# Optimization experiments

Measured on AMD Instinct MI355X. Metric: run time of the kernel, lower is better.

Reference implementation:

```python
import jax, jax.numpy as jnp
import numpy as np

D = 512
NPRE = NMLP = NPOST = 16
TOPK = 8
P = NPRE * NMLP * NPOST
HMAX = 5 * D  # max MLP expert hidden (j//4 up to 3 -> 2+3=5)
B, S = 1, 256


def _gelu(x):
    return jax.nn.gelu(x, approximate=False)  # torch nn.GELU default (erf)


def _ln(x, g, b, eps=1e-5):
    m = x.mean(-1, keepdims=True)
    v = ((x - m) ** 2).mean(-1, keepdims=True)
    return (x - m) / jnp.sqrt(v + eps) * g + b


def setup_inputs() -> dict:
    key = jax.random.key(0)
    ks = iter(jax.random.split(key, 16))
    w = lambda shape: jax.random.normal(next(ks), shape, jnp.float32) * 0.02
    inp = {"x": jax.random.normal(next(ks), (B, S, D), jnp.float32)}
    # router: Linear(D,256)->GELU->Linear(256,128)->GELU->Linear(128,P); dropout off (eval)
    inp["Wr1"] = w((D, 256)); inp["br1"] = jnp.zeros((256,), jnp.float32)
    inp["Wr2"] = w((256, 128)); inp["br2"] = jnp.zeros((128,), jnp.float32)
    inp["Wr3"] = w((128, P)); inp["br3"] = jnp.zeros((P,), jnp.float32)
    inp["temp"] = jnp.ones((1,), jnp.float32)
    # pre experts: Linear(D,D) + LayerNorm + {GELU,ReLU,Tanh} by i%3
    inp["Wpre"] = w((NPRE, D, D)); inp["bpre"] = jnp.zeros((NPRE, D), jnp.float32)
    inp["gpre"] = jnp.ones((NPRE, D), jnp.float32); inp["bpre_ln"] = jnp.zeros((NPRE, D), jnp.float32)
    # mlp experts: heterogeneous hidden D*(2+j//4), zero-padded to HMAX
    W1 = np.zeros((NMLP, D, HMAX), np.float32)
    b1 = np.zeros((NMLP, HMAX), np.float32)
    W2 = np.zeros((NMLP, HMAX, D), np.float32)
    rng = np.random.default_rng(0)
    for j in range(NMLP):
        h = D * (2 + j // 4)
        W1[j, :, :h] = rng.normal(0.0, 0.02, (D, h)).astype(np.float32)
        W2[j, :h, :] = rng.normal(0.0, 0.02, (h, D)).astype(np.float32)
    inp["W1"] = jnp.asarray(W1); inp["b1"] = jnp.asarray(b1)
    inp["W2"] = jnp.asarray(W2); inp["b2"] = jnp.zeros((NMLP, D), jnp.float32)
    # post experts: Linear(D,D) + (LayerNorm if p%2==0); dropout off (eval)
    inp["Wpost"] = w((NPOST, D, D)); inp["bpost"] = jnp.zeros((NPOST, D), jnp.float32)
    inp["gpost"] = jnp.ones((NPOST, D), jnp.float32); inp["bpost_ln"] = jnp.zeros((NPOST, D), jnp.float32)
    return inp


def _forward(x, Wr1, br1, Wr2, br2, Wr3, br3, temp,
             Wpre, bpre, gpre, bpre_ln, W1, b1, W2, b2,
             Wpost, bpost, gpost, bpost_ln):
    b, s, _ = x.shape
    # ---- router ----
    h = _gelu(x @ Wr1 + br1)
    h = _gelu(h @ Wr2 + br2)
    scores = h @ Wr3 + br3  # [B,S,P]
    # ---- GLBL loss (torch.var -> unbiased, ddof=1) ----
    freq = jax.nn.softmax(scores, axis=-1).mean((0, 1))  # [P]
    var = jnp.sum((freq - freq.mean()) ** 2) / (P - 1)
    glbl_loss = P * var
    # ---- top-k routing ----
    probs = jax.nn.softmax(scores / temp, axis=-1)
    top_vals, top_idx = jax.lax.top_k(probs, TOPK)  # [B,S,K]
    bb = jnp.arange(b)[:, None, None]
    ss = jnp.arange(s)[None, :, None]
    pw = jnp.zeros_like(probs).at[bb, ss, top_idx].set(top_vals)
    pw = pw / (pw.sum(-1, keepdims=True) + 1e-8)  # diagnostic pathway_weights
    # ---- decompose pathway index -> (pre, mlp, post) ----
    pre_i = top_idx // (NMLP * NPOST)
    rem = top_idx % (NMLP * NPOST)
    mlp_i = rem // NPOST
    post_i = rem % NPOST
    # ---- pre experts: compute all, gather per slot ----
    pre_lin = jnp.einsum('bsd,edf->bsef', x, Wpre) + bpre  # [B,S,E,D]
    pre_ln = _ln(pre_lin, gpre, bpre_ln)
    aid = (jnp.arange(NPRE) % 3)[:, None]  # [E,1] broadcast over D
    pre_all = jnp.where(aid == 0, _gelu(pre_ln),
                        jnp.where(aid == 1, jax.nn.relu(pre_ln), jnp.tanh(pre_ln)))
    x_pre = jnp.take_along_axis(pre_all, pre_i[..., None], axis=2)  # [B,S,K,D]
    # ---- mlp experts: heterogeneous hidden, dense compute + mask-combine ----
    mlp_out = jnp.zeros_like(x_pre)
    for j in range(NMLP):
        hd = D * (2 + j // 4)
        hj = x_pre @ W1[j, :, :hd] + b1[j, :hd]
        hj = _gelu(hj) if j % 2 == 0 else jax.nn.relu(hj)
        yj = hj @ W2[j, :hd, :] + b2[j]
        mlp_out = mlp_out + jnp.where((mlp_i == j)[..., None], yj, 0.0)
    # ---- post experts ----
    post_out = jnp.zeros_like(mlp_out)
    for p in range(NPOST):
        yp = mlp_out @ Wpost[p] + bpost[p]
        if p % 2 == 0:
            yp = _ln(yp, gpost[p], bpost_ln[p])
        post_out = post_out + jnp.where((post_i == p)[..., None], yp, 0.0)
    # ---- weighted sum over slots (original uses raw top-k probs as weights) ----
    output = jnp.einsum('bsk,bskd->bsd', top_vals, post_out)
    return output, glbl_loss, pw


def reference(x, Wr1, br1, Wr2, br2, Wr3, br3, temp,
              Wpre, bpre, gpre, bpre_ln, W1, b1, W2, b2,
              Wpost, bpost, gpost, bpost_ln):
    return _forward(x, Wr1, br1, Wr2, br2, Wr3, br3, temp,
                    Wpre, bpre, gpre, bpre_ln, W1, b1, W2, b2,
                    Wpost, bpost, gpost, bpost_ln)
```

## Files before the change

### kernel.cpp

```cpp
#include <hip/hip_runtime.h>
#include <math.h>

#define S 256
#define D 512
#define P 4096
#define TOPK 8
#define NPAIR (S*TOPK)
#define HMAX 2560

#define OFF_H1     0
#define OFF_H2     65536
#define OFF_SCORES 98304
#define OFF_PROBS  1146880
#define OFF_TOPV   2195456
#define OFF_TOPI   2197504
#define OFF_CNT    2199552
#define OFF_LP     2199616
#define OFF_LM     2232384
#define OFF_LQ     2265152
#define OFF_PRE    2297920
#define OFF_HBUF   3346496
#define OFF_MLPO   8589376
#define OFF_POSTL  9637952
#define OFF_FREQ   10686528


__device__ __forceinline__ float geluf(float x) {
    return 0.5f * x * (1.0f + erff(x * 0.70710678118654752440f));
}

__device__ __forceinline__ float blockReduceSum(float v, float* red, int tid) {
    __syncthreads();
    #pragma unroll
    for (int o = 32; o; o >>= 1) v += __shfl_down(v, o);
    if ((tid & 63) == 0) red[tid >> 6] = v;
    __syncthreads();
    return red[0] + red[1] + red[2] + red[3];
}

__device__ __forceinline__ float blockReduceMax(float v, float* red, int tid) {
    __syncthreads();
    #pragma unroll
    for (int o = 32; o; o >>= 1) v = fmaxf(v, __shfl_down(v, o));
    if ((tid & 63) == 0) red[tid >> 6] = v;
    __syncthreads();
    return fmaxf(fmaxf(red[0], red[1]), fmaxf(red[2], red[3]));
}

__global__ __launch_bounds__(256) void gemm_grouped(
    const float* __restrict__ A, int lda, int amode,
    const int* __restrict__ list, int listStride,
    const int* __restrict__ counts, int fixedM,
    const float* __restrict__ W, long long wStride, int ldw,
    const float* __restrict__ bias, int biasStride,
    float* __restrict__ C, int ldc,
    int N, int K, int hetN, int hetK, int act)
{
    int e = blockIdx.z;
    int he = 512 * (2 + (e >> 2));
    int Ne = hetN ? he : N;
    int Ke = hetK ? he : K;
    int Me = counts ? counts[e] : fixedM;
    int row0 = blockIdx.y * 64; if (row0 >= Me) return;
    int col0 = blockIdx.x * 64; if (col0 >= Ne) return;

    const float* We = W + (long long)e * wStride + col0;
    const float* be = bias + (size_t)e * biasStride + col0;
    const int* le = list ? (list + (size_t)e * listStride) : nullptr;

    __shared__ float As[64][36];
    __shared__ float Ws[32][68];

    int tid = threadIdx.x;
    int laR = tid >> 3, laK = (tid & 7) << 2;
    int lwK = tid >> 4, lwC = (tid & 15) << 2;

    const float* aptr0 = nullptr; const float* aptr1 = nullptr;
    {
        int r = row0 + laR;
        if (r < Me) { int ri = le ? le[r] : r; if (amode) ri >>= 3; aptr0 = A + (size_t)ri * lda + laK; }
        r = row0 + laR + 32;
        if (r < Me) { int ri = le ? le[r] : r; if (amode) ri >>= 3; aptr1 = A + (size_t)ri * lda + laK; }
    }

    float acc[4][4] = {};
    int tr = (tid >> 4) << 2, tc = (tid & 15) << 2;

    for (int k0 = 0; k0 < Ke; k0 += 32) {
        float4 v0 = make_float4(0.f, 0.f, 0.f, 0.f);
        float4 v1 = v0;
        if (aptr0) v0 = *(const float4*)(aptr0 + k0);
        if (aptr1) v1 = *(const float4*)(aptr1 + k0);
        *(float4*)&As[laR][laK] = v0;
        *(float4*)&As[laR + 32][laK] = v1;

        float4 w0 = *(const float4*)(We + (size_t)(k0 + lwK) * ldw + lwC);
        float4 w1 = *(const float4*)(We + (size_t)(k0 + lwK + 16) * ldw + lwC);
        *(float4*)&Ws[lwK][lwC] = w0;
        *(float4*)&Ws[lwK + 16][lwC] = w1;
        __syncthreads();

        #pragma unroll
        for (int kk = 0; kk < 32; kk++) {
            float a0 = As[tr][kk], a1 = As[tr + 1][kk], a2 = As[tr + 2][kk], a3 = As[tr + 3][kk];
            float b0 = Ws[kk][tc], b1 = Ws[kk][tc + 1], b2 = Ws[kk][tc + 2], b3 = Ws[kk][tc + 3];
            acc[0][0] += a0 * b0; acc[0][1] += a0 * b1; acc[0][2] += a0 * b2; acc[0][3] += a0 * b3;
            acc[1][0] += a1 * b0; acc[1][1] += a1 * b1; acc[1][2] += a1 * b2; acc[1][3] += a1 * b3;
            acc[2][0] += a2 * b0; acc[2][1] += a2 * b1; acc[2][2] += a2 * b2; acc[2][3] += a2 * b3;
            acc[3][0] += a3 * b0; acc[3][1] += a3 * b1; acc[3][2] += a3 * b2; acc[3][3] += a3 * b3;
        }
        __syncthreads();
    }

    int ae = act;
    if (act == 3) ae = (e & 1) ? 2 : 1;
    #pragma unroll
    for (int i = 0; i < 4; i++) {
        int r = row0 + tr + i;
        if (r >= Me) continue;
        int crow = le ? le[r] : r;
        float* Cr = C + (size_t)crow * ldc + col0 + tc;
        #pragma unroll
        for (int j = 0; j < 4; j++) {
            float v = acc[i][j] + be[tc + j];
            if (ae == 1) v = geluf(v);
            else if (ae == 2) v = fmaxf(v, 0.f);
            Cr[j] = v;
        }
    }
}

__global__ __launch_bounds__(256) void softmax_topk_kernel(
    const float* __restrict__ scores, const float* __restrict__ temp,
    float* __restrict__ probs, float* __restrict__ topv, int* __restrict__ topi,
    float* __restrict__ pw)
{
    __shared__ float s[P];
    __shared__ float red[8];
    __shared__ float lv[256];
    __shared__ int   li[256];
    __shared__ float tvS[TOPK];
    __shared__ int   tiS[TOPK];

    int t = blockIdx.x, tid = threadIdx.x;
    const float* srow = scores + (size_t)t * P;

    float loc[16];
    #pragma unroll
    for (int j = 0; j < 16; j++) { loc[j] = srow[tid + 256 * j]; }

    float m = -1e30f;
    #pragma unroll
    for (int j = 0; j < 16; j++) m = fmaxf(m, loc[j]);
    m = blockReduceMax(m, red, tid);

    float invT = 1.0f / temp[0];
    float p1[16], pT[16];
    float s1 = 0.f, sT = 0.f;
    #pragma unroll
    for (int j = 0; j < 16; j++) {
        float d = loc[j] - m;
        p1[j] = expf(d);        s1 += p1[j];
        pT[j] = expf(d * invT); sT += pT[j];
    }
    s1 = blockReduceSum(s1, red, tid);
    sT = blockReduceSum(sT, red, tid);

    float iZ1 = 1.f / s1;
    float* prow = probs + (size_t)t * P;
    float* pwrow = pw + (size_t)t * P;
    #pragma unroll
    for (int j = 0; j < 16; j++) {
        int i = tid + 256 * j;
        prow[i] = p1[j] * iZ1;
        s[i] = pT[j];
        pwrow[i] = 0.f;
    }
    __syncthreads();

    for (int it = 0; it < TOPK; it++) {
        float bv = -1e30f; int bi = -1;
        #pragma unroll
        for (int j = 0; j < 16; j++) {
            int i = tid + 256 * j;
            float v = s[i];
            if (v > bv) { bv = v; bi = i; }
        }
        lv[tid] = bv; li[tid] = bi;
        __syncthreads();
        for (int st = 128; st; st >>= 1) {
            if (tid < st) {
                float ov = lv[tid + st]; int oi = li[tid + st];
                if (ov > lv[tid] || (ov == lv[tid] && oi < li[tid])) { lv[tid] = ov; li[tid] = oi; }
            }
            __syncthreads();
        }
        if (tid == 0) { tvS[it] = lv[0]; tiS[it] = li[0]; s[li[0]] = -1e30f; }
        __syncthreads();
    }

    if (tid == 0) {
        float iZT = 1.f / sT;
        float tvn[TOPK]; float ssum = 0.f;
        #pragma unroll
        for (int it = 0; it < TOPK; it++) { tvn[it] = tvS[it] * iZT; ssum += tvn[it]; }
        float inv = 1.f / (ssum + 1e-8f);
        #pragma unroll
        for (int it = 0; it < TOPK; it++) {
            int pair = t * TOPK + it;
            topv[pair] = tvn[it];
            topi[pair] = tiS[it];
            pwrow[tiS[it]] = tvn[it] * inv;
        }
    }
}

__global__ void freq_kernel(const float* __restrict__ probs, float* __restrict__ freq) {
    int p = blockIdx.x * 256 + threadIdx.x;
    float sum = 0.f;
    for (int t = 0; t < S; t++) sum += probs[(size_t)t * P + p];
    freq[p] = sum * (1.f / (float)S);
}

__global__ __launch_bounds__(256) void glbl_kernel(const float* __restrict__ freq, float* __restrict__ outLoss) {
    __shared__ float red[8];
    int tid = threadIdx.x;
    float sum = 0.f;
    #pragma unroll
    for (int j = 0; j < 16; j++) sum += freq[tid + 256 * j];
    float tot = blockReduceSum(sum, red, tid);
    float mean = tot * (1.f / (float)P);
    float q = 0.f;
    #pragma unroll
    for (int j = 0; j < 16; j++) { float d = freq[tid + 256 * j] - mean; q += d * d; }
    float sq = blockReduceSum(q, red, tid);
    if (tid == 0) outLoss[0] = (float)P * (sq / (float)(P - 1));
}

__global__ void zero_cnt_kernel(int* cnt) {
    if (threadIdx.x < 64) cnt[threadIdx.x] = 0;
}

__global__ void build_lists_kernel(const int* __restrict__ topi, int* cnt,
                                   int* lp, int* lm, int* lq) {
    int pair = blockIdx.x * 256 + threadIdx.x;
    if (pair >= NPAIR) return;
    int idx = topi[pair];
    int pre = idx >> 8, rem = idx & 255, ml = rem >> 4, po = rem & 15;
    int pos;
    pos = atomicAdd(&cnt[pre], 1);      lp[pre * NPAIR + pos] = pair;
    pos = atomicAdd(&cnt[16 + ml], 1);  lm[ml * NPAIR + pos] = pair;
    pos = atomicAdd(&cnt[32 + po], 1);  lq[po * NPAIR + pos] = pair;
}

__global__ __launch_bounds__(256) void pre_lnact_kernel(
    float* __restrict__ preOut, const int* __restrict__ topi,
    const float* __restrict__ g, const float* __restrict__ b)
{
    __shared__ float red[8];
    int pair = blockIdx.x, tid = threadIdx.x;
    int e = topi[pair] >> 8;
    float* row = preOut + (size_t)pair * D;
    float v0 = row[tid], v1 = row[tid + 256];
    float sm = blockReduceSum(v0 + v1, red, tid) * (1.f / (float)D);
    float d0 = v0 - sm, d1 = v1 - sm;
    float vv = blockReduceSum(d0 * d0 + d1 * d1, red, tid) * (1.f / (float)D);
    float rs = rsqrtf(vv + 1e-5f);
    v0 = d0 * rs * g[e * D + tid]       + b[e * D + tid];
    v1 = d1 * rs * g[e * D + tid + 256] + b[e * D + tid + 256];
    int a = e % 3;
    if (a == 0)      { v0 = geluf(v0);      v1 = geluf(v1); }
    else if (a == 1) { v0 = fmaxf(v0, 0.f); v1 = fmaxf(v1, 0.f); }
    else             { v0 = tanhf(v0);      v1 = tanhf(v1); }
    row[tid] = v0; row[tid + 256] = v1;
}

__global__ __launch_bounds__(256) void combine_kernel(
    const float* __restrict__ postLin, const float* __restrict__ topv,
    const int* __restrict__ topi, const float* __restrict__ g,
    const float* __restrict__ b, float* __restrict__ out)
{
    __shared__ float red[8];
    int t = blockIdx.x, tid = threadIdx.x;
    float a0 = 0.f, a1 = 0.f;
    for (int sl = 0; sl < TOPK; sl++) {
        int pair = t * TOPK + sl;
        int e = topi[pair] & 15;
        float tv = topv[pair];
        const float* row = postLin + (size_t)pair * D;
        float v0 = row[tid], v1 = row[tid + 256];
        if ((e & 1) == 0) {
            float sm = blockReduceSum(v0 + v1, red, tid) * (1.f / (float)D);
            float d0 = v0 - sm, d1 = v1 - sm;
            float vv = blockReduceSum(d0 * d0 + d1 * d1, red, tid) * (1.f / (float)D);
            float rs = rsqrtf(vv + 1e-5f);
            v0 = d0 * rs * g[e * D + tid]       + b[e * D + tid];
            v1 = d1 * rs * g[e * D + tid + 256] + b[e * D + tid + 256];
        }
        a0 += tv * v0; a1 += tv * v1;
    }
    out[(size_t)t * D + tid] = a0;
    out[(size_t)t * D + tid + 256] = a1;
}

extern "C" void kernel_launch(void* const* d_in, const int* in_sizes, int n_in,
                              void* d_out, int out_size, void* d_ws, size_t ws_size,
                              hipStream_t stream) {
    const float* x    = (const float*)d_in[0];
    const float* Wr1  = (const float*)d_in[1];
    const float* br1  = (const float*)d_in[2];
    const float* Wr2  = (const float*)d_in[3];
    const float* br2  = (const float*)d_in[4];
    const float* Wr3  = (const float*)d_in[5];
    const float* br3  = (const float*)d_in[6];
    const float* temp = (const float*)d_in[7];
    const float* Wpre = (const float*)d_in[8];
    const float* bpre = (const float*)d_in[9];
    const float* gpre = (const float*)d_in[10];
    const float* bpre_ln = (const float*)d_in[11];
    const float* W1   = (const float*)d_in[12];
    const float* b1   = (const float*)d_in[13];
    const float* W2   = (const float*)d_in[14];
    const float* b2   = (const float*)d_in[15];
    const float* Wpost = (const float*)d_in[16];
    const float* bpost = (const float*)d_in[17];
    const float* gpost = (const float*)d_in[18];
    const float* bpost_ln = (const float*)d_in[19];

    float* ws = (float*)d_ws;
    float* h1     = ws + OFF_H1;
    float* h2     = ws + OFF_H2;
    float* scores = ws + OFF_SCORES;
    float* probs  = ws + OFF_PROBS;
    float* topv   = ws + OFF_TOPV;
    int*   topi   = (int*)(ws + OFF_TOPI);
    int*   cnt    = (int*)(ws + OFF_CNT);
    int*   lp     = (int*)(ws + OFF_LP);
    int*   lm     = (int*)(ws + OFF_LM);
    int*   lq     = (int*)(ws + OFF_LQ);
    float* preOut = ws + OFF_PRE;
    float* Hbuf   = ws + OFF_HBUF;
    float* mlpOut = ws + OFF_MLPO;
    float* postLin = ws + OFF_POSTL;
    float* freq   = ws + OFF_FREQ;

    float* out   = (float*)d_out;
    float* outLoss = out + S * D;
    float* pw    = out + S * D + 1;

    hipLaunchKernelGGL(zero_cnt_kernel, dim3(1), dim3(64), 0, stream, cnt);

    hipLaunchKernelGGL(gemm_grouped, dim3(4, 4, 1), dim3(256), 0, stream,
        x, D, 0, (const int*)nullptr, 0, (const int*)nullptr, S,
        Wr1, 0LL, 256, br1, 0, h1, 256, 256, 512, 0, 0, 1);
    hipLaunchKernelGGL(gemm_grouped, dim3(2, 4, 1), dim3(256), 0, stream,
        h1, 256, 0, (const int*)nullptr, 0, (const int*)nullptr, S,
        Wr2, 0LL, 128, br2, 0, h2, 128, 128, 256, 0, 0, 1);
    hipLaunchKernelGGL(gemm_grouped, dim3(64, 4, 1), dim3(256), 0, stream,
        h2, 128, 0, (const int*)nullptr, 0, (const int*)nullptr, S,
        Wr3, 0LL, P, br3, 0, scores, P, P, 128, 0, 0, 0);

    hipLaunchKernelGGL(softmax_topk_kernel, dim3(S), dim3(256), 0, stream,
        scores, temp, probs, topv, topi, pw);

    hipLaunchKernelGGL(freq_kernel, dim3(16), dim3(256), 0, stream, probs, freq);
    hipLaunchKernelGGL(glbl_kernel, dim3(1), dim3(256), 0, stream, freq, outLoss);

    hipLaunchKernelGGL(build_lists_kernel, dim3(8), dim3(256), 0, stream, topi, cnt, lp, lm, lq);

    hipLaunchKernelGGL(gemm_grouped, dim3(8, 32, 16), dim3(256), 0, stream,
        x, D, 1, lp, NPAIR, cnt, 0,
        Wpre, (long long)D * D, D, bpre, D, preOut, D, D, D, 0, 0, 0);
    hipLaunchKernelGGL(pre_lnact_kernel, dim3(NPAIR), dim3(256), 0, stream,
        preOut, topi, gpre, bpre_ln);

    hipLaunchKernelGGL(gemm_grouped, dim3(40, 32, 16), dim3(256), 0, stream,
        preOut, D, 0, lm, NPAIR, cnt + 16, 0,
        W1, (long long)D * HMAX, HMAX, b1, HMAX, Hbuf, HMAX, 0, D, 1, 0, 3);
    hipLaunchKernelGGL(gemm_grouped, dim3(8, 32, 16), dim3(256), 0, stream,
        Hbuf, HMAX, 0, lm, NPAIR, cnt + 16, 0,
        W2, (long long)HMAX * D, D, b2, D, mlpOut, D, D, 0, 0, 1, 0);

    hipLaunchKernelGGL(gemm_grouped, dim3(8, 32, 16), dim3(256), 0, stream,
        mlpOut, D, 0, lq, NPAIR, cnt + 32, 0,
        Wpost, (long long)D * D, D, bpost, D, postLin, D, D, D, 0, 0, 0);

    hipLaunchKernelGGL(combine_kernel, dim3(S), dim3(256), 0, stream,
        postLin, topv, topi, gpost, bpost_ln, out);
}
```

Measured before the change: 773.6 us.

## Rewrite grouped GEMM with persistent work queue, async LDS double buffering, fused freq

```diff
diff --git a/kernel.cpp b/kernel.cpp
--- a/kernel.cpp
+++ b/kernel.cpp
@@ -11,24 +11,34 @@
 #define OFF_H1     0
 #define OFF_H2     65536
 #define OFF_SCORES 98304
-#define OFF_PROBS  1146880
-#define OFF_TOPV   2195456
-#define OFF_TOPI   2197504
-#define OFF_CNT    2199552
-#define OFF_LP     2199616
-#define OFF_LM     2232384
-#define OFF_LQ     2265152
-#define OFF_PRE    2297920
-#define OFF_HBUF   3346496
-#define OFF_MLPO   8589376
-#define OFF_POSTL  9637952
-#define OFF_FREQ   10686528
+#define OFF_TOPV   1146880
+#define OFF_TOPI   1148928
+#define OFF_CNT    1150976
+#define OFF_LP     1151040
+#define OFF_LM     1183808
+#define OFF_LQ     1216576
+#define OFF_PRE    1249344
+#define OFF_HBUF   2297920
+#define OFF_MLPO   7540800
+#define OFF_POSTL  8589376
+#define OFF_FREQ   9637952
+#define OFF_NIT    9642048
+#define OFF_QPRE   9642052
+#define OFF_QM1    9644100
+#define OFF_QM2    9652292
+#define OFF_QPOST  9654340
 
 
 __device__ __forceinline__ float geluf(float x) {
     return 0.5f * x * (1.0f + erff(x * 0.70710678118654752440f));
 }
 
+__device__ __forceinline__ void async_copy16(float* lds, const float* g) {
+    __builtin_amdgcn_global_load_lds(
+        (const __attribute__((address_space(1))) unsigned int*)g,
+        (__attribute__((address_space(3))) unsigned int*)lds, 16, 0, 0);
+}
+
 __device__ __forceinline__ float blockReduceSum(float v, float* red, int tid) {
     __syncthreads();
     #pragma unroll
@@ -47,92 +57,134 @@
     return fmaxf(fmaxf(red[0], red[1]), fmaxf(red[2], red[3]));
 }
 
-__global__ __launch_bounds__(256) void gemm_grouped(
+__global__ __launch_bounds__(256) void gemm_tile(
     const float* __restrict__ A, int lda, int amode,
-    const int* __restrict__ list, int listStride,
-    const int* __restrict__ counts, int fixedM,
+    const int* __restrict__ lists, const int* __restrict__ cnt,
+    const int4* __restrict__ queue, const int* __restrict__ nItemsPtr, int stageIdx,
+    int denseNB, int denseM,
     const float* __restrict__ W, long long wStride, int ldw,
     const float* __restrict__ bias, int biasStride,
-    float* __restrict__ C, int ldc,
-    int N, int K, int hetN, int hetK, int act)
+    float* __restrict__ C, int ldc, int K, int hetK, int act)
 {
-    int e = blockIdx.z;
-    int he = 512 * (2 + (e >> 2));
-    int Ne = hetN ? he : N;
-    int Ke = hetK ? he : K;
-    int Me = counts ? counts[e] : fixedM;
-    int row0 = blockIdx.y * 64; if (row0 >= Me) return;
-    int col0 = blockIdx.x * 64; if (col0 >= Ne) return;
-
-    const float* We = W + (long long)e * wStride + col0;
-    const float* be = bias + (size_t)e * biasStride + col0;
-    const int* le = list ? (list + (size_t)e * listStride) : nullptr;
-
-    __shared__ float As[64][36];
-    __shared__ float Ws[32][68];
-
-    int tid = threadIdx.x;
-    int laR = tid >> 3, laK = (tid & 7) << 2;
-    int lwK = tid >> 4, lwC = (tid & 15) << 2;
-
-    const float* aptr0 = nullptr; const float* aptr1 = nullptr;
-    {
-        int r = row0 + laR;
-        if (r < Me) { int ri = le ? le[r] : r; if (amode) ri >>= 3; aptr0 = A + (size_t)ri * lda + laK; }
-        r = row0 + laR + 32;
-        if (r < Me) { int ri = le ? le[r] : r; if (amode) ri >>= 3; aptr1 = A + (size_t)ri * lda + laK; }
-    }
-
-    float acc[4][4] = {};
-    int tr = (tid >> 4) << 2, tc = (tid & 15) << 2;
-
-    for (int k0 = 0; k0 < Ke; k0 += 32) {
-        float4 v0 = make_float4(0.f, 0.f, 0.f, 0.f);
-        float4 v1 = v0;
-        if (aptr0) v0 = *(const float4*)(aptr0 + k0);
-        if (aptr1) v1 = *(const float4*)(aptr1 + k0);
-        *(float4*)&As[laR][laK] = v0;
-        *(float4*)&As[laR + 32][laK] = v1;
-
-        float4 w0 = *(const float4*)(We + (size_t)(k0 + lwK) * ldw + lwC);
-        float4 w1 = *(const float4*)(We + (size_t)(k0 + lwK + 16) * ldw + lwC);
-        *(float4*)&Ws[lwK][lwC] = w0;
-        *(float4*)&Ws[lwK + 16][lwC] = w1;
+    __shared__ float As[2][32][68];
+    __shared__ float Bs[2][32][64];
+    __shared__ int rAs[64];
+    __shared__ int rC[64];
+
+    int t = threadIdx.x;
+    int wid = t >> 6;
+    int lane = t & 63;
+    int tr4 = (t >> 4) << 2;
+    int tc4 = (t & 15) << 2;
+
+    int nWork = queue ? nItemsPtr[stageIdx] : (denseNB * ((denseM + 63) >> 6));
+
+    for (int w = blockIdx.x; w < nWork; w += gridDim.x) {
+        int e, m0, n0, Me;
+        if (queue) {
+            int4 it = queue[w];
+            e = it.x; m0 = it.y; n0 = it.z;
+            Me = cnt[e];
+        } else {
+            e = 0; m0 = (w / denseNB) * 64; n0 = (w % denseNB) * 64; Me = denseM;
+        }
+        int Ke = hetK ? (512 * (2 + (e >> 2))) : K;
+        const float* We = W + (long long)e * wStride + n0;
+        const int* le = lists ? (lists + (size_t)e * NPAIR) : nullptr;
+
         __syncthreads();
-
+        if (t < 64) {
+            int r = m0 + t;
+            int ar, cr;
+            if (le) {
+                int rr = (r < Me) ? r : (Me - 1);
+                int pair = le[rr];
+                ar = amode ? (pair >> 3) : pair;
+                cr = (r < Me) ? pair : -1;
+            } else { ar = r; cr = r; }
+            rAs[t] = ar; rC[t] = cr;
+        }
+        __syncthreads();
+
+        int aRow = rAs[lane];
+        const float* aBase = A + (size_t)aRow * lda + (wid << 3);
+        const float* bBase = We + (size_t)(wid * 8 + (lane >> 4)) * ldw + ((lane & 15) << 2);
+        float* bDst0 = &Bs[0][wid * 8][0];
+        float* bDst1 = &Bs[1][wid * 8][0];
+
+        float acc[4][4] = {};
+        float4 av0, av1;
+
+        av0 = *(const float4*)(aBase + 0);
+        av1 = *(const float4*)(aBase + 4);
+        {
+            const float* g = bBase;
+            async_copy16(bDst0, g);
+            async_copy16(bDst0 + 256, g + (size_t)4 * ldw);
+        }
         #pragma unroll
-        for (int kk = 0; kk < 32; kk++) {
-            float a0 = As[tr][kk], a1 = As[tr + 1][kk], a2 = As[tr + 2][kk], a3 = As[tr + 3][kk];
-            float b0 = Ws[kk][tc], b1 = Ws[kk][tc + 1], b2 = Ws[kk][tc + 2], b3 = Ws[kk][tc + 3];
-            acc[0][0] += a0 * b0; acc[0][1] += a0 * b1; acc[0][2] += a0 * b2; acc[0][3] += a0 * b3;
-            acc[1][0] += a1 * b0; acc[1][1] += a1 * b1; acc[1][2] += a1 * b2; acc[1][3] += a1 * b3;
-            acc[2][0] += a2 * b0; acc[2][1] += a2 * b1; acc[2][2] += a2 * b2; acc[2][3] += a2 * b3;
-            acc[3][0] += a3 * b0; acc[3][1] += a3 * b1; acc[3][2] += a3 * b2; acc[3][3] += a3 * b3;
-        }
+        for (int j = 0; j < 4; j++) As[0][(wid << 3) + j][lane] = ((const float*)&av0)[j];
+        #pragma unroll
+        for (int j = 0; j < 4; j++) As[0][(wid << 3) + 4 + j][lane] = ((const float*)&av1)[j];
         __syncthreads();
-    }
-
-    int ae = act;
-    if (act == 3) ae = (e & 1) ? 2 : 1;
-    #pragma unroll
-    for (int i = 0; i < 4; i++) {
-        int r = row0 + tr + i;
-        if (r >= Me) continue;
-        int crow = le ? le[r] : r;
-        float* Cr = C + (size_t)crow * ldc + col0 + tc;
-        #pragma unroll
-        for (int j = 0; j < 4; j++) {
-            float v = acc[i][j] + be[tc + j];
-            if (ae == 1) v = geluf(v);
-            else if (ae == 2) v = fmaxf(v, 0.f);
-            Cr[j] = v;
+
+        int nk = Ke >> 5;
+        int buf = 0;
+        for (int ks = 0; ks < nk; ks++) {
+            bool more = (ks + 1) < nk;
+            if (more) {
+                int k0 = (ks + 1) << 5;
+                av0 = *(const float4*)(aBase + k0);
+                av1 = *(const float4*)(aBase + k0 + 4);
+                const float* g = bBase + (size_t)k0 * ldw;
+                float* bd = buf ? bDst0 : bDst1;
+                async_copy16(bd, g);
+                async_copy16(bd + 256, g + (size_t)4 * ldw);
+            }
+            #pragma unroll
+            for (int kk = 0; kk < 32; kk++) {
+                float4 a = *(const float4*)&As[buf][kk][tr4];
+                float4 b = *(const float4*)&Bs[buf][kk][tc4];
+                acc[0][0] += a.x * b.x; acc[0][1] += a.x * b.y; acc[0][2] += a.x * b.z; acc[0][3] += a.x * b.w;
+                acc[1][0] += a.y * b.x; acc[1][1] += a.y * b.y; acc[1][2] += a.y * b.z; acc[1][3] += a.y * b.w;
+                acc[2][0] += a.z * b.x; acc[2][1] += a.z * b.y; acc[2][2] += a.z * b.z; acc[2][3] += a.z * b.w;
+                acc[3][0] += a.w * b.x; acc[3][1] += a.w * b.y; acc[3][2] += a.w * b.z; acc[3][3] += a.w * b.w;
+            }
+            if (more) {
+                int nb = buf ^ 1;
+                #pragma unroll
+                for (int j = 0; j < 4; j++) As[nb][(wid << 3) + j][lane] = ((const float*)&av0)[j];
+                #pragma unroll
+                for (int j = 0; j < 4; j++) As[nb][(wid << 3) + 4 + j][lane] = ((const float*)&av1)[j];
+            }
+            __syncthreads();
+            buf ^= 1;
+        }
+
+        {
+            const float* be = bias + (size_t)e * biasStride + n0 + tc4;
+            float4 b4 = *(const float4*)be;
+            int ae = (act == 3) ? ((e & 1) ? 2 : 1) : act;
+            #pragma unroll
+            for (int i = 0; i < 4; i++) {
+                int cr = rC[tr4 + i];
+                if (cr < 0) continue;
+                float v0 = acc[i][0] + b4.x;
+                float v1 = acc[i][1] + b4.y;
+                float v2 = acc[i][2] + b4.z;
+                float v3 = acc[i][3] + b4.w;
+                if (ae == 1) { v0 = geluf(v0); v1 = geluf(v1); v2 = geluf(v2); v3 = geluf(v3); }
+                else if (ae == 2) { v0 = fmaxf(v0, 0.f); v1 = fmaxf(v1, 0.f); v2 = fmaxf(v2, 0.f); v3 = fmaxf(v3, 0.f); }
+                float4 v = make_float4(v0, v1, v2, v3);
+                *(float4*)(C + (size_t)cr * ldc + n0 + tc4) = v;
+            }
         }
     }
 }
 
 __global__ __launch_bounds__(256) void softmax_topk_kernel(
     const float* __restrict__ scores, const float* __restrict__ temp,
-    float* __restrict__ probs, float* __restrict__ topv, int* __restrict__ topi,
+    float* __restrict__ freq, float* __restrict__ topv, int* __restrict__ topi,
     float* __restrict__ pw)
 {
     __shared__ float s[P];
@@ -166,13 +218,12 @@
     s1 = blockReduceSum(s1, red, tid);
     sT = blockReduceSum(sT, red, tid);
 
-    float iZ1 = 1.f / s1;
-    float* prow = probs + (size_t)t * P;
+    float scale1 = (1.f / s1) * (1.f / (float)S);
     float* pwrow = pw + (size_t)t * P;
     #pragma unroll
     for (int j = 0; j < 16; j++) {
         int i = tid + 256 * j;
-        prow[i] = p1[j] * iZ1;
+        atomicAdd(&freq[i], p1[j] * scale1);
         s[i] = pT[j];
         pwrow[i] = 0.f;
     }
@@ -215,13 +266,6 @@
     }
 }
 
-__global__ void freq_kernel(const float* __restrict__ probs, float* __restrict__ freq) {
-    int p = blockIdx.x * 256 + threadIdx.x;
-    float sum = 0.f;
-    for (int t = 0; t < S; t++) sum += probs[(size_t)t * P + p];
-    freq[p] = sum * (1.f / (float)S);
-}
-
 __global__ __launch_bounds__(256) void glbl_kernel(const float* __restrict__ freq, float* __restrict__ outLoss) {
     __shared__ float red[8];
     int tid = threadIdx.x;
@@ -237,8 +281,10 @@
     if (tid == 0) outLoss[0] = (float)P * (sq / (float)(P - 1));
 }
 
-__global__ void zero_cnt_kernel(int* cnt) {
-    if (threadIdx.x < 64) cnt[threadIdx.x] = 0;
+__global__ void zero_misc_kernel(int* cnt, float* freq) {
+    int t = threadIdx.x;
+    if (t < 64) cnt[t] = 0;
+    for (int i = t; i < P; i += 256) freq[i] = 0.f;
 }
 
 __global__ void build_lists_kernel(const int* __restrict__ topi, int* cnt,
@@ -251,6 +297,42 @@
     pos = atomicAdd(&cnt[pre], 1);      lp[pre * NPAIR + pos] = pair;
     pos = atomicAdd(&cnt[16 + ml], 1);  lm[ml * NPAIR + pos] = pair;
     pos = atomicAdd(&cnt[32 + po], 1);  lq[po * NPAIR + pos] = pair;
+}
+
+__global__ void build_queue_kernel(const int* __restrict__ cnt,
+                                   int4* qpre, int4* qm1, int4* qm2, int4* qpost,
+                                   int* nItems) {
+    __shared__ int ccount[64];
+    __shared__ int coff[64];
+    int t = threadIdx.x;
+    int s = t >> 4, e = t & 15;
+    if (t < 64) {
+        int base = (s == 0) ? 0 : (s == 3) ? 32 : 16;
+        int me = cnt[base + e];
+        int nm = (me + 63) >> 6;
+        int nb = (s == 1) ? (8 * (2 + (e >> 2))) : 8;
+        ccount[t] = nm * nb;
+    }
+    __syncthreads();
+    if (t == 0) {
+        for (int ss = 0; ss < 4; ss++) {
+            int run = 0;
+            for (int i = 0; i < 16; i++) { coff[ss * 16 + i] = run; run += ccount[ss * 16 + i]; }
+            nItems[ss] = run;
+        }
+    }
+    __syncthreads();
+    if (t < 64) {
+        int base = (s == 0) ? 0 : (s == 3) ? 32 : 16;
+        int me = cnt[base + e];
+        int nm = (me + 63) >> 6;
+        int nb = (s == 1) ? (8 * (2 + (e >> 2))) : 8;
+        int4* q = (s == 0) ? qpre : (s == 1) ? qm1 : (s == 2) ? qm2 : qpost;
+        int off = coff[t];
+        for (int mb = 0; mb < nm; mb++)
+            for (int nbk = 0; nbk < nb; nbk++)
+                q[off++] = make_int4(e, mb * 64, nbk * 64, 0);
+    }
 }
 
 __global__ __launch_bounds__(256) void pre_lnact_kernel(
@@ -328,62 +410,68 @@
     const float* bpost_ln = (const float*)d_in[19];
 
     float* ws = (float*)d_ws;
-    float* h1     = ws + OFF_H1;
-    float* h2     = ws + OFF_H2;
-    float* scores = ws + OFF_SCORES;
-    float* probs  = ws + OFF_PROBS;
-    float* topv   = ws + OFF_TOPV;
-    int*   topi   = (int*)(ws + OFF_TOPI);
-    int*   cnt    = (int*)(ws + OFF_CNT);
-    int*   lp     = (int*)(ws + OFF_LP);
-    int*   lm     = (int*)(ws + OFF_LM);
-    int*   lq     = (int*)(ws + OFF_LQ);
-    float* preOut = ws + OFF_PRE;
-    float* Hbuf   = ws + OFF_HBUF;
-    float* mlpOut = ws + OFF_MLPO;
+    float* h1      = ws + OFF_H1;
+    float* h2      = ws + OFF_H2;
+    float* scores  = ws + OFF_SCORES;
+    float* topv    = ws + OFF_TOPV;
+    int*   topi    = (int*)(ws + OFF_TOPI);
+    int*   cnt     = (int*)(ws + OFF_CNT);
+    int*   lp      = (int*)(ws + OFF_LP);
+    int*   lm      = (int*)(ws + OFF_LM);
+    int*   lq      = (int*)(ws + OFF_LQ);
+    float* preOut  = ws + OFF_PRE;
+    float* Hbuf    = ws + OFF_HBUF;
+    float* mlpOut  = ws + OFF_MLPO;
     float* postLin = ws + OFF_POSTL;
-    float* freq   = ws + OFF_FREQ;
-
-    float* out   = (float*)d_out;
+    float* freq    = ws + OFF_FREQ;
+    int*   nit     = (int*)(ws + OFF_NIT);
+    int4*  qpre    = (int4*)(ws + OFF_QPRE);
+    int4*  qm1     = (int4*)(ws + OFF_QM1);
+    int4*  qm2     = (int4*)(ws + OFF_QM2);
+    int4*  qpost   = (int4*)(ws + OFF_QPOST);
+
+    float* out     = (float*)d_out;
     float* outLoss = out + S * D;
-    float* pw    = out + S * D + 1;
-
-    hipLaunchKernelGGL(zero_cnt_kernel, dim3(1), dim3(64), 0, stream, cnt);
-
-    hipLaunchKernelGGL(gemm_grouped, dim3(4, 4, 1), dim3(256), 0, stream,
-        x, D, 0, (const int*)nullptr, 0, (const int*)nullptr, S,
-        Wr1, 0LL, 256, br1, 0, h1, 256, 256, 512, 0, 0, 1);
-    hipLaunchKernelGGL(gemm_grouped, dim3(2, 4, 1), dim3(256), 0, stream,
-        h1, 256, 0, (const int*)nullptr, 0, (const int*)nullptr, S,
-        Wr2, 0LL, 128, br2, 0, h2, 128, 128, 256, 0, 0, 1);
-    hipLaunchKernelGGL(gemm_grouped, dim3(64, 4, 1), dim3(256), 0, stream,
-        h2, 128, 0, (const int*)nullptr, 0, (const int*)nullptr, S,
-        Wr3, 0LL, P, br3, 0, scores, P, P, 128, 0, 0, 0);
+    float* pw      = out + S * D + 1;
+
+    hipLaunchKernelGGL(zero_misc_kernel, dim3(1), dim3(256), 0, stream, cnt, freq);
+
+    hipLaunchKernelGGL(gemm_tile, dim3(16), dim3(256), 0, stream,
+        x, D, 0, (const int*)nullptr, (const int*)nullptr,
+        (const int4*)nullptr, (const int*)nullptr, 0, 4, S,
+        Wr1, 0LL, 256, br1, 0, h1, 256, 512, 0, 1);
+    hipLaunchKernelGGL(gemm_tile, dim3(8), dim3(256), 0, stream,
+        h1, 256, 0, (const int*)nullptr, (const int*)nullptr,
+        (const int4*)nullptr, (const int*)nullptr, 0, 2, S,
+        Wr2, 0LL, 128, br2, 0, h2, 128, 256, 0, 1);
+    hipLaunchKernelGGL(gemm_tile, dim3(256), dim3(256), 0, stream,
+        h2, 128, 0, (const int*)nullptr, (const int*)nullptr,
+        (const int4*)nullptr, (const int*)nullptr, 0, 64, S,
+        Wr3, 0LL, P, br3, 0, scores, P, 128, 0, 0);
 
     hipLaunchKernelGGL(softmax_topk_kernel, dim3(S), dim3(256), 0, stream,
-        scores, temp, probs, topv, topi, pw);
-
-    hipLaunchKernelGGL(freq_kernel, dim3(16), dim3(256), 0, stream, probs, freq);
+        scores, temp, freq, topv, topi, pw);
     hipLaunchKernelGGL(glbl_kernel, dim3(1), dim3(256), 0, stream, freq, outLoss);
 
     hipLaunchKernelGGL(build_lists_kernel, dim3(8), dim3(256), 0, stream, topi, cnt, lp, lm, lq);
-
-    hipLaunchKernelGGL(gemm_grouped, dim3(8, 32, 16), dim3(256), 0, stream,
-        x, D, 1, lp, NPAIR, cnt, 0,
-        Wpre, (long long)D * D, D, bpre, D, preOut, D, D, D, 0, 0, 0);
+    hipLaunchKernelGGL(build_queue_kernel, dim3(1), dim3(256), 0, stream, cnt, qpre, qm1, qm2, qpost, nit);
+
+    hipLaunchKernelGGL(gemm_tile, dim3(512), dim3(256), 0, stream,
+        x, D, 1, lp, cnt, qpre, nit, 0, 0, 0,
+        Wpre, (long long)D * D, D, bpre, D, preOut, D, 512, 0, 0);
     hipLaunchKernelGGL(pre_lnact_kernel, dim3(NPAIR), dim3(256), 0, stream,
         preOut, topi, gpre, bpre_ln);
 
-    hipLaunchKernelGGL(gemm_grouped, dim3(40, 32, 16), dim3(256), 0, stream,
-        preOut, D, 0, lm, NPAIR, cnt + 16, 0,
-        W1, (long long)D * HMAX, HMAX, b1, HMAX, Hbuf, HMAX, 0, D, 1, 0, 3);
-    hipLaunchKernelGGL(gemm_grouped, dim3(8, 32, 16), dim3(256), 0, stream,
-        Hbuf, HMAX, 0, lm, NPAIR, cnt + 16, 0,
-        W2, (long long)HMAX * D, D, b2, D, mlpOut, D, D, 0, 0, 1, 0);
-
-    hipLaunchKernelGGL(gemm_grouped, dim3(8, 32, 16), dim3(256), 0, stream,
-        mlpOut, D, 0, lq, NPAIR, cnt + 32, 0,
-        Wpost, (long long)D * D, D, bpost, D, postLin, D, D, D, 0, 0, 0);
+    hipLaunchKernelGGL(gemm_tile, dim3(1024), dim3(256), 0, stream,
+        preOut, D, 0, lm, cnt + 16, qm1, nit, 1, 0, 0,
+        W1, (long long)D * HMAX, HMAX, b1, HMAX, Hbuf, HMAX, 512, 0, 3);
+    hipLaunchKernelGGL(gemm_tile, dim3(512), dim3(256), 0, stream,
+        Hbuf, HMAX, 0, lm, cnt + 16, qm2, nit, 2, 0, 0,
+        W2, (long long)HMAX * D, D, b2, D, mlpOut, D, 0, 1, 0);
+
+    hipLaunchKernelGGL(gemm_tile, dim3(512), dim3(256), 0, stream,
+        mlpOut, D, 0, lq, cnt + 32, qpost, nit, 3, 0, 0,
+        Wpost, (long long)D * D, D, bpost, D, postLin, D, 512, 0, 0);
 
     hipLaunchKernelGGL(combine_kernel, dim3(S), dim3(256), 0, stream,
         postLin, topv, topi, gpost, bpost_ln, out);
```

New measurement: 724.8 us. 1.07x faster.
